# Performance work log

Measured on AMD Instinct MI355X. Metric: run time of the kernel, lower is better.

The kernel has to match this reference:

```python
import jax, jax.numpy as jnp
import numpy as np

B, S, HID = 1, 2048, 2048
NH = 16
D_NOPE, D_ROPE, D_V = 128, 64, 128
D_QK = D_NOPE + D_ROPE            # 192
KV_R = 512                        # kv_lora_rank
EPS = 1e-6
SCALING = D_QK ** -0.5
NEG = -1e9


def rms_norm(x, w):
    xf = x.astype(jnp.float32)
    var = jnp.mean(xf * xf, axis=-1, keepdims=True)
    return w * (xf * jax.lax.rsqrt(var + EPS)).astype(x.dtype)


def rotate_half(x):
    x1, x2 = jnp.split(x, 2, axis=-1)
    return jnp.concatenate([-x2, x1], axis=-1)


def deinterleave(x):
    # torch: view(..., d//2, 2).transpose(-1, -2).reshape(..., d)
    # => [x0, x2, x4, ..., x1, x3, x5, ...]
    return jnp.concatenate([x[..., 0::2], x[..., 1::2]], axis=-1)


def setup_inputs() -> dict:
    key = jax.random.key(0)
    ks = jax.random.split(key, 6)
    hidden_states = jax.random.normal(ks[0], (B, S, HID), jnp.float32)
    # rotary cos/sin over qk_rope_head_dim
    inv_freq = 1.0 / (10000.0 ** (np.arange(0, D_ROPE, 2, dtype=np.float32) / D_ROPE))
    freqs = np.outer(np.arange(S, dtype=np.float32), inv_freq)   # [S, D_ROPE/2]
    emb = np.concatenate([freqs, freqs], axis=-1)                # [S, D_ROPE]
    cos = jnp.asarray(np.cos(emb), jnp.float32)[None]            # [1, S, D_ROPE]
    sin = jnp.asarray(np.sin(emb), jnp.float32)[None]
    # additive causal mask [1, 1, S, S]
    causal = np.where(np.tril(np.ones((S, S), dtype=bool)), 0.0, NEG).astype(np.float32)
    attention_mask = jnp.asarray(causal)[None, None]
    sc = lambda k, shp: jax.random.normal(k, shp, jnp.float32) * (shp[-1] ** -0.5)
    q_proj_w = sc(ks[1], (NH * D_QK, HID))
    kv_a_proj_w = sc(ks[2], (KV_R + D_ROPE, HID))
    kv_a_ln_w = jnp.ones((KV_R,), jnp.float32)
    kv_b_proj_w = sc(ks[3], (NH * (D_NOPE + D_V), KV_R))
    o_proj_w = sc(ks[4], (HID, NH * D_V))
    return dict(hidden_states=hidden_states, cos=cos, sin=sin,
                attention_mask=attention_mask, q_proj_w=q_proj_w,
                kv_a_proj_w=kv_a_proj_w, kv_a_ln_w=kv_a_ln_w,
                kv_b_proj_w=kv_b_proj_w, o_proj_w=o_proj_w)


def reference(hidden_states, cos, sin, attention_mask,
              q_proj_w, kv_a_proj_w, kv_a_ln_w, kv_b_proj_w, o_proj_w):
    b, s, _ = hidden_states.shape
    # Q projection -> [b, NH, s, D_QK]
    q = (hidden_states @ q_proj_w.T).reshape(b, s, NH, D_QK).transpose(0, 2, 1, 3)
    q_pass, q_rot = q[..., :D_NOPE], q[..., D_NOPE:]
    # compressed KV + shared rope key
    ckv = hidden_states @ kv_a_proj_w.T                           # [b, s, KV_R + D_ROPE]
    k_pass_c, k_rot = ckv[..., :KV_R], ckv[..., KV_R:]
    kv = (rms_norm(k_pass_c, kv_a_ln_w) @ kv_b_proj_w.T)
    kv = kv.reshape(b, s, NH, D_NOPE + D_V).transpose(0, 2, 1, 3)  # [b, NH, s, .]
    k_pass, value_states = kv[..., :D_NOPE], kv[..., D_NOPE:]
    k_rot = k_rot.reshape(b, 1, s, D_ROPE)
    # interleaved RoPE (rope_interleave=True)
    q_rot = deinterleave(q_rot)
    k_rot = deinterleave(k_rot)
    c = cos[:, None]  # [1, 1, s, D_ROPE]
    sn = sin[:, None]
    q_rot = q_rot * c + rotate_half(q_rot) * sn
    k_rot = k_rot * c + rotate_half(k_rot) * sn
    k_rot = jnp.broadcast_to(k_rot, (b, NH, s, D_ROPE))
    query_states = jnp.concatenate([q_pass, q_rot], axis=-1)      # [b, NH, s, D_QK]
    key_states = jnp.concatenate([k_pass, k_rot], axis=-1)
    # eager attention (num_key_value_groups == 1)
    scores = jnp.einsum('bhqd,bhkd->bhqk', query_states, key_states) * SCALING
    scores = scores + attention_mask[:, :, :, :s]
    attn = jax.nn.softmax(scores.astype(jnp.float32), axis=-1).astype(query_states.dtype)
    attn_out = jnp.einsum('bhqk,bhkd->bhqd', attn, value_states)  # [b, NH, s, D_V]
    attn_out = attn_out.transpose(0, 2, 1, 3).reshape(b, s, NH * D_V)
    return attn_out @ o_proj_w.T
```

## Files before the change

### kernel.cpp

```cpp
#include <hip/hip_runtime.h>
#include <hip/hip_bf16.h>
#include <stdint.h>
#include <stddef.h>

#define S_LEN 2048
#define HID_DIM 2048
#define NH 16
#define D_QK 192
#define D_NOPE 128
#define D_ROPE 64
#define D_V 128
#define KV_R 512
#define CKV_N (KV_R + D_ROPE)
#define KVB_N (NH * (D_NOPE + D_V))
#define QN (NH * D_QK)
#define CAT_N (QN + CKV_N)
#define SCALING 0.07216878364870322f

typedef __attribute__((ext_vector_type(8))) short short8;
typedef __attribute__((ext_vector_type(4))) short short4v;
typedef __attribute__((ext_vector_type(4))) float f32x4;

__device__ __forceinline__ short f2bf_bits(float f) {
  unsigned u = __float_as_uint(f);
  unsigned r = (u + 0x7fffu + ((u >> 16) & 1u)) >> 16;
  return (short)(r & 0xffffu);
}
__device__ __forceinline__ float bf2f(short b) {
  return __uint_as_float(((unsigned)(unsigned short)b) << 16);
}

__device__ __forceinline__ f32x4 mfma_bf16(short8 a, short8 b, f32x4 c) {
  return __builtin_amdgcn_mfma_f32_16x16x32_bf16(a, b, c, 0, 0, 0);
}

__global__ __launch_bounds__(256)
void cvt5_k(const float* __restrict__ s0, short* __restrict__ d0, int c0,
            const float* __restrict__ s1, short* __restrict__ d1, int c1,
            const float* __restrict__ s2, short* __restrict__ d2, int c2,
            const float* __restrict__ s3, short* __restrict__ d3, int c3,
            const float* __restrict__ s4, short* __restrict__ d4, int c4) {
  const int i = blockIdx.x * 256 + threadIdx.x;
  const float* s; short* d; int base;
  if      (i < c0) { s = s0; d = d0; base = 0;  }
  else if (i < c1) { s = s1; d = d1; base = c0; }
  else if (i < c2) { s = s2; d = d2; base = c1; }
  else if (i < c3) { s = s3; d = d3; base = c2; }
  else if (i < c4) { s = s4; d = d4; base = c3; }
  else return;
  const int j = i - base;
  const float4 v = ((const float4*)s)[j];
  short4v o;
  o.x = f2bf_bits(v.x); o.y = f2bf_bits(v.y);
  o.z = f2bf_bits(v.z); o.w = f2bf_bits(v.w);
  ((short4v*)d)[j] = o;
}

template <bool OUTF32>
__global__ __launch_bounds__(256, 3)
void gemm_bt(const short* __restrict__ A, const short* __restrict__ B,
             void* __restrict__ Cv, int M, int N, int K) {
  __shared__ short sA[2][128 * 32];
  __shared__ short sB[2][128 * 32];
  const int tid  = threadIdx.x;
  const int wave = tid >> 6;
  const int lane = tid & 63;
  const int bm = blockIdx.y * 128;
  const int bn = blockIdx.x * 128;
  const int wr = wave >> 1, wc = wave & 1;
  const int fr = lane & 15, fk = (lane >> 4) * 8;
  const int srow = lane >> 2;
  const int scol = (lane & 3) * 8;

  f32x4 acc[4][4];
  for (int i = 0; i < 4; ++i)
    for (int j = 0; j < 4; ++j)
      for (int r = 0; r < 4; ++r) acc[i][j][r] = 0.f;

  for (int k0 = 0; k0 < K; k0 += 64) {
    __syncthreads();
#pragma unroll
    for (int cc = 0; cc < 2; ++cc) {
      const int c = wave * 2 + cc;
      const int ar = bm + c * 16 + srow;
      int br = bn + c * 16 + srow; if (br > N - 1) br = N - 1;
#pragma unroll
      for (int kh = 0; kh < 2; ++kh) {
        __builtin_amdgcn_global_load_lds(
            (const __attribute__((address_space(1))) void*)(A + (size_t)ar * K + k0 + kh * 32 + scol),
            (__attribute__((address_space(3))) void*)(sA[kh] + c * 512), 16, 0, 0);
        __builtin_amdgcn_global_load_lds(
            (const __attribute__((address_space(1))) void*)(B + (size_t)br * K + k0 + kh * 32 + scol),
            (__attribute__((address_space(3))) void*)(sB[kh] + c * 512), 16, 0, 0);
      }
    }
    __syncthreads();
#pragma unroll
    for (int kh = 0; kh < 2; ++kh) {
      short8 af[4], bfr[4];
#pragma unroll
      for (int i = 0; i < 4; ++i)
        af[i] = *(const short8*)(sA[kh] + (wr * 64 + i * 16 + fr) * 32 + fk);
#pragma unroll
      for (int j = 0; j < 4; ++j)
        bfr[j] = *(const short8*)(sB[kh] + (wc * 64 + j * 16 + fr) * 32 + fk);
#pragma unroll
      for (int i = 0; i < 4; ++i)
#pragma unroll
        for (int j = 0; j < 4; ++j)
          acc[i][j] = mfma_bf16(af[i], bfr[j], acc[i][j]);
    }
  }

  const int cr = (lane >> 4) * 4, ccol = lane & 15;
#pragma unroll
  for (int i = 0; i < 4; ++i)
#pragma unroll
    for (int j = 0; j < 4; ++j) {
      const int col = bn + wc * 64 + j * 16 + ccol;
      if (col < N) {
#pragma unroll
        for (int r = 0; r < 4; ++r) {
          const int row = bm + wr * 64 + i * 16 + cr + r;
          if (OUTF32)
            ((float*)Cv)[(size_t)row * N + col] = acc[i][j][r];
          else
            ((short*)Cv)[(size_t)row * N + col] = f2bf_bits(acc[i][j][r]);
        }
      }
    }
}

__global__ __launch_bounds__(256)
void rmsnorm_k(const short* __restrict__ qckv, const float* __restrict__ w,
               short* __restrict__ out) {
  const int s = blockIdx.x, t = threadIdx.x;
  const short* x = qckv + (size_t)s * CAT_N + QN;
  float v0 = bf2f(x[2 * t]), v1 = bf2f(x[2 * t + 1]);
  float ss = v0 * v0 + v1 * v1;
#pragma unroll
  for (int off = 1; off < 64; off <<= 1) ss += __shfl_xor(ss, off, 64);
  __shared__ float red[4];
  if ((t & 63) == 0) red[t >> 6] = ss;
  __syncthreads();
  const float tot = red[0] + red[1] + red[2] + red[3];
  const float sc = rsqrtf(tot * (1.0f / 512.0f) + 1e-6f);
  out[(size_t)s * KV_R + 2 * t]     = f2bf_bits(v0 * sc * w[2 * t]);
  out[(size_t)s * KV_R + 2 * t + 1] = f2bf_bits(v1 * sc * w[2 * t + 1]);
}

__global__ __launch_bounds__(256)
void prep_k(const short* __restrict__ qckv, const short* __restrict__ kvb,
            const float* __restrict__ cosb, const float* __restrict__ sinb,
            short* __restrict__ Qs, short* __restrict__ Ks) {
  const int s = blockIdx.x, t = threadIdx.x;
  const short* qrow = qckv + (size_t)s * CAT_N;
  __shared__ float cs[32], sn[32];
  __shared__ short krs[64];
  if (t < 32) {
    const float c  = cosb[(size_t)s * 64 + t];
    const float si = sinb[(size_t)s * 64 + t];
    cs[t] = c; sn[t] = si;
    const float e0 = bf2f(qrow[QN + KV_R + 2 * t]);
    const float e1 = bf2f(qrow[QN + KV_R + 2 * t + 1]);
    krs[t]      = f2bf_bits(e0 * c - e1 * si);
    krs[t + 32] = f2bf_bits(e1 * c + e0 * si);
  }
  __syncthreads();
  const int h = t >> 4, i = t & 15;
  *(short8*)(Qs + ((size_t)h * S_LEN + s) * D_QK + i * 8) =
      *(const short8*)(qrow + h * D_QK + i * 8);
  *(short8*)(Ks + ((size_t)h * S_LEN + s) * D_QK + i * 8) =
      *(const short8*)(kvb + (size_t)s * KVB_N + h * 256 + i * 8);
#pragma unroll
  for (int p = 0; p < 2; ++p) {
    const int ii = i * 2 + p;
    const float e0 = bf2f(qrow[h * D_QK + 128 + 2 * ii]);
    const float e1 = bf2f(qrow[h * D_QK + 128 + 2 * ii + 1]);
    Qs[((size_t)h * S_LEN + s) * D_QK + 128 + ii] = f2bf_bits(e0 * cs[ii] - e1 * sn[ii]);
    Qs[((size_t)h * S_LEN + s) * D_QK + 160 + ii] = f2bf_bits(e1 * cs[ii] + e0 * sn[ii]);
  }
#pragma unroll
  for (int p = 0; p < 4; ++p) {
    const int idx = t * 4 + p;
    const int hh = idx >> 6, ii = idx & 63;
    Ks[((size_t)hh * S_LEN + s) * D_QK + 128 + ii] = krs[ii];
  }
}

__global__ __launch_bounds__(256)
void vtr_k(const short* __restrict__ kvb, short* __restrict__ Vt) {
  const int st = blockIdx.x, dt = blockIdx.y, h = blockIdx.z;
  __shared__ short sT[64][72];
  const int id = threadIdx.x;
#pragma unroll
  for (int p = 0; p < 2; ++p) {
    const int q = id + p * 256;
    const int row = q >> 3, c8 = q & 7;
    *(short8*)(&sT[row][c8 * 8]) =
        *(const short8*)(kvb + (size_t)(st * 64 + row) * KVB_N + h * 256 + 128 + dt * 64 + c8 * 8);
  }
  __syncthreads();
#pragma unroll
  for (int p = 0; p < 2; ++p) {
    const int q = id + p * 256;
    const int drow = q >> 3, c8 = q & 7;
    short8 o;
#pragma unroll
    for (int j = 0; j < 8; ++j) o[j] = sT[c8 * 8 + j][drow];
    *(short8*)(Vt + ((size_t)h * D_V + dt * 64 + drow) * S_LEN + st * 64 + c8 * 8) = o;
  }
}

__global__ __launch_bounds__(256, 2)
void flash_k(const short* __restrict__ Qs, const short* __restrict__ Ks,
             const short* __restrict__ Vt, short* __restrict__ Oc) {
  __shared__ short sK[64 * 200];
  __shared__ short sVt[128 * 72];
  __shared__ short P_lds[4][16 * 72];
  const int tid = threadIdx.x;
  const int wv = tid >> 6;
  const int lane = tid & 63;
  const int blk = blockIdx.x;
  const int h = ((blk & 7) << 1) | ((blk >> 3) & 1);
  const int a = blk >> 4;
  const int b = 31 - a;
  const int fr = lane & 15, g = lane >> 4;
  const int q0[2] = { a * 64 + wv * 16, b * 64 + wv * 16 };

  const short* Qh = Qs + (size_t)h * S_LEN * D_QK;
  const short* Kh = Ks + (size_t)h * S_LEN * D_QK;
  const short* Vh = Vt + (size_t)h * D_V * S_LEN;

  short8 qa[2][6];
#pragma unroll
  for (int rt = 0; rt < 2; ++rt)
#pragma unroll
    for (int c = 0; c < 6; ++c)
      qa[rt][c] = *(const short8*)(Qh + (size_t)(q0[rt] + fr) * D_QK + c * 32 + g * 8);

  f32x4 o[2][8];
  float m_i[2][4], l_i[2][4];
#pragma unroll
  for (int rt = 0; rt < 2; ++rt)
#pragma unroll
    for (int r = 0; r < 4; ++r) {
      m_i[rt][r] = -1e30f; l_i[rt][r] = 0.f;
#pragma unroll
      for (int f = 0; f < 8; ++f) o[rt][f][r] = 0.f;
    }

  short* pl = &P_lds[wv][0];
  const int jn = b + 1;
  for (int jt = 0; jt < jn; ++jt) {
    const int j0 = jt << 6;
    const bool lightOn = (jt <= a);
    __syncthreads();
    short8 kc[6], vc[4];
#pragma unroll
    for (int p = 0; p < 6; ++p) {
      const int id = tid + p * 256;
      const int row = id / 24, c8 = id % 24;
      kc[p] = *(const short8*)(Kh + (size_t)(j0 + row) * D_QK + c8 * 8);
    }
#pragma unroll
    for (int p = 0; p < 4; ++p) {
      const int id = tid + p * 256;
      const int row = id >> 3, c8 = id & 7;
      vc[p] = *(const short8*)(Vh + (size_t)row * S_LEN + j0 + c8 * 8);
    }
#pragma unroll
    for (int p = 0; p < 6; ++p) {
      const int id = tid + p * 256;
      const int row = id / 24, c8 = id % 24;
      *(short8*)(sK + row * 200 + c8 * 8) = kc[p];
    }
#pragma unroll
    for (int p = 0; p < 4; ++p) {
      const int id = tid + p * 256;
      const int row = id >> 3, c8 = id & 7;
      *(short8*)(sVt + row * 72 + c8 * 8) = vc[p];
    }
    __syncthreads();

    f32x4 sc[2][4];
#pragma unroll
    for (int rt = 0; rt < 2; ++rt)
#pragma unroll
      for (int t = 0; t < 4; ++t)
        for (int r = 0; r < 4; ++r) sc[rt][t][r] = -1e30f;
#pragma unroll
    for (int t = 0; t < 4; ++t) {
      const bool hOn = (j0 + t * 16 <= q0[1] + 15);
      const bool lOn = lightOn && (j0 + t * 16 <= q0[0] + 15);
      if (hOn || lOn) {
        short8 kfr[6];
#pragma unroll
        for (int c = 0; c < 6; ++c)
          kfr[c] = *(const short8*)(sK + (t * 16 + fr) * 200 + c * 32 + g * 8);
        if (lOn) {
          f32x4 acc; for (int r = 0; r < 4; ++r) acc[r] = 0.f;
#pragma unroll
          for (int c = 0; c < 6; ++c) acc = mfma_bf16(qa[0][c], kfr[c], acc);
          sc[0][t] = acc;
        }
        if (hOn) {
          f32x4 acc; for (int r = 0; r < 4; ++r) acc[r] = 0.f;
#pragma unroll
          for (int c = 0; c < 6; ++c) acc = mfma_bf16(qa[1][c], kfr[c], acc);
          sc[1][t] = acc;
        }
      }
    }

#pragma unroll
    for (int rt = 0; rt < 2; ++rt) {
      if (rt == 0 && !lightOn) continue;
      const int qq = q0[rt];
      float tm[4];
#pragma unroll
      for (int r = 0; r < 4; ++r) {
        const int row = qq + g * 4 + r;
        float mx = -1e30f;
#pragma unroll
        for (int t = 0; t < 4; ++t) {
          const float v = (j0 + t * 16 + fr <= row) ? sc[rt][t][r] * SCALING : -1e30f;
          sc[rt][t][r] = v;
          mx = fmaxf(mx, v);
        }
        tm[r] = mx;
      }
#pragma unroll
      for (int off = 1; off < 16; off <<= 1)
#pragma unroll
        for (int r = 0; r < 4; ++r)
          tm[r] = fmaxf(tm[r], __shfl_xor(tm[r], off, 16));
      float ps[4];
#pragma unroll
      for (int r = 0; r < 4; ++r) {
        const float mnew = fmaxf(m_i[rt][r], tm[r]);
        const float alpha = __expf(m_i[rt][r] - mnew);
        m_i[rt][r] = mnew;
        l_i[rt][r] *= alpha;
        float s = 0.f;
#pragma unroll
        for (int t = 0; t < 4; ++t) {
          const float p = __expf(sc[rt][t][r] - mnew);
          sc[rt][t][r] = p;
          s += p;
        }
        ps[r] = s;
#pragma unroll
        for (int f = 0; f < 8; ++f) o[rt][f][r] *= alpha;
      }
#pragma unroll
      for (int off = 1; off < 16; off <<= 1)
#pragma unroll
        for (int r = 0; r < 4; ++r)
          ps[r] += __shfl_xor(ps[r], off, 16);
#pragma unroll
      for (int r = 0; r < 4; ++r) l_i[rt][r] += ps[r];

#pragma unroll
      for (int r = 0; r < 4; ++r)
#pragma unroll
        for (int t = 0; t < 4; ++t)
          pl[(g * 4 + r) * 72 + t * 16 + fr] = f2bf_bits(sc[rt][t][r]);
      __builtin_amdgcn_fence(__ATOMIC_ACQ_REL, "wavefront");
      const short8 pa0 = *(const short8*)(pl + fr * 72 + g * 8);
      const short8 pa1 = *(const short8*)(pl + fr * 72 + 32 + g * 8);
#pragma unroll
      for (int f = 0; f < 8; ++f) {
        const short* vr = sVt + (f * 16 + fr) * 72 + g * 8;
        const short8 vb0 = *(const short8*)(vr);
        const short8 vb1 = *(const short8*)(vr + 32);
        o[rt][f] = mfma_bf16(pa1, vb1, mfma_bf16(pa0, vb0, o[rt][f]));
      }
    }
  }

#pragma unroll
  for (int rt = 0; rt < 2; ++rt)
#pragma unroll
    for (int r = 0; r < 4; ++r) {
      const float inv = 1.0f / l_i[rt][r];
      const int row = q0[rt] + g * 4 + r;
#pragma unroll
      for (int f = 0; f < 8; ++f)
        Oc[(size_t)row * (NH * D_V) + h * D_V + f * 16 + fr] = f2bf_bits(o[rt][f][r] * inv);
    }
}

extern "C" void kernel_launch(void* const* d_in, const int* in_sizes, int n_in,
                              void* d_out, int out_size, void* d_ws, size_t ws_size,
                              hipStream_t stream) {
  const float* hidden = (const float*)d_in[0];
  const float* cosb   = (const float*)d_in[1];
  const float* sinb   = (const float*)d_in[2];
  const float* q_w    = (const float*)d_in[4];
  const float* kva_w  = (const float*)d_in[5];
  const float* ln_w   = (const float*)d_in[6];
  const float* kvb_w  = (const float*)d_in[7];
  const float* o_w    = (const float*)d_in[8];
  float* out = (float*)d_out;

  char* ws = (char*)d_ws;
  size_t off = 0;
  auto alloc = [&](size_t elems) {
    short* p = (short*)(ws + off);
    off += ((elems * 2 + 255) & ~(size_t)255);
    return p;
  };
  short* hid_b   = alloc((size_t)S_LEN * HID_DIM);
  short* qkva_wb = alloc((size_t)CAT_N * HID_DIM);
  short* kvb_wb  = alloc((size_t)KVB_N * KV_R);
  short* o_wb    = alloc((size_t)HID_DIM * NH * D_V);
  short* qckv    = alloc((size_t)S_LEN * CAT_N);
  short* ckvn    = alloc((size_t)S_LEN * KV_R);
  short* kvb     = alloc((size_t)S_LEN * KVB_N);
  short* Qs      = alloc((size_t)NH * S_LEN * D_QK);
  short* Ks      = alloc((size_t)NH * S_LEN * D_QK);
  short* Vt      = alloc((size_t)NH * D_V * S_LEN);
  short* Oc      = alloc((size_t)S_LEN * NH * D_V);

  dim3 blk(256);
  const int n0 = (S_LEN * HID_DIM) / 4;
  const int n1 = (QN * HID_DIM) / 4;
  const int n2 = (CKV_N * HID_DIM) / 4;
  const int n3 = (KVB_N * KV_R) / 4;
  const int n4e = (HID_DIM * NH * D_V) / 4;
  const int c0 = n0, c1 = c0 + n1, c2 = c1 + n2, c3 = c2 + n3, c4 = c3 + n4e;
  cvt5_k<<<dim3((c4 + 255) / 256), blk, 0, stream>>>(
      hidden, hid_b, c0,
      q_w, qkva_wb, c1,
      kva_w, qkva_wb + (size_t)QN * HID_DIM, c2,
      kvb_w, kvb_wb, c3,
      o_w, o_wb, c4);

  gemm_bt<false><<<dim3((CAT_N + 127) / 128, S_LEN / 128), blk, 0, stream>>>(
      hid_b, qkva_wb, qckv, S_LEN, CAT_N, HID_DIM);
  rmsnorm_k<<<dim3(S_LEN), blk, 0, stream>>>(qckv, ln_w, ckvn);
  gemm_bt<false><<<dim3(KVB_N / 128, S_LEN / 128), blk, 0, stream>>>(
      ckvn, kvb_wb, kvb, S_LEN, KVB_N, KV_R);
  prep_k<<<dim3(S_LEN), blk, 0, stream>>>(qckv, kvb, cosb, sinb, Qs, Ks);
  vtr_k<<<dim3(S_LEN / 64, D_V / 64, NH), blk, 0, stream>>>(kvb, Vt);
  flash_k<<<dim3(NH * 16), blk, 0, stream>>>(Qs, Ks, Vt, Oc);
  gemm_bt<true><<<dim3(HID_DIM / 128, S_LEN / 128), blk, 0, stream>>>(
      Oc, o_wb, out, S_LEN, HID_DIM, NH * D_V);
}
```

Measured before the change: 320.1 us.

## Prefetch next K/V tile into registers during flash attention compute

Issues the global loads for the next K and V tiles into registers right after the shared-memory barrier, so they are in flight while the current tile's QK^T, softmax and PV run. The following iteration only copies those registers into LDS. Per-thread row and column indices are precomputed once, and launch bounds drop from 2 to 1 blocks per CU so the extra live registers do not cause spills. The cost is lower occupancy, which may hide latency less well than running two blocks per CU.

```diff
diff --git a/kernel.cpp b/kernel.cpp
--- a/kernel.cpp
+++ b/kernel.cpp
@@ -212,7 +212,7 @@
   }
 }
 
-__global__ __launch_bounds__(256, 2)
+__global__ __launch_bounds__(256, 1)
 void flash_k(const short* __restrict__ Qs, const short* __restrict__ Ks,
              const short* __restrict__ Vt, short* __restrict__ Oc) {
   __shared__ short sK[64 * 200];
@@ -232,6 +232,18 @@
   const short* Kh = Ks + (size_t)h * S_LEN * D_QK;
   const short* Vh = Vt + (size_t)h * D_V * S_LEN;
 
+  int rowK[6], c8K[6], rowV[4], c8V[4];
+#pragma unroll
+  for (int p = 0; p < 6; ++p) {
+    const int id = tid + p * 256;
+    rowK[p] = id / 24; c8K[p] = id % 24;
+  }
+#pragma unroll
+  for (int p = 0; p < 4; ++p) {
+    const int id = tid + p * 256;
+    rowV[p] = id >> 3; c8V[p] = id & 7;
+  }
+
   short8 qa[2][6];
 #pragma unroll
   for (int rt = 0; rt < 2; ++rt)
@@ -249,6 +261,14 @@
 #pragma unroll
       for (int f = 0; f < 8; ++f) o[rt][f][r] = 0.f;
     }
+
+  short8 kc[6], vc[4];
+#pragma unroll
+  for (int p = 0; p < 6; ++p)
+    kc[p] = *(const short8*)(Kh + (size_t)rowK[p] * D_QK + c8K[p] * 8);
+#pragma unroll
+  for (int p = 0; p < 4; ++p)
+    vc[p] = *(const short8*)(Vh + (size_t)rowV[p] * S_LEN + c8V[p] * 8);
 
   short* pl = &P_lds[wv][0];
   const int jn = b + 1;
@@ -256,32 +276,22 @@
     const int j0 = jt << 6;
     const bool lightOn = (jt <= a);
     __syncthreads();
-    short8 kc[6], vc[4];
-#pragma unroll
-    for (int p = 0; p < 6; ++p) {
-      const int id = tid + p * 256;
-      const int row = id / 24, c8 = id % 24;
-      kc[p] = *(const short8*)(Kh + (size_t)(j0 + row) * D_QK + c8 * 8);
-    }
-#pragma unroll
-    for (int p = 0; p < 4; ++p) {
-      const int id = tid + p * 256;
-      const int row = id >> 3, c8 = id & 7;
-      vc[p] = *(const short8*)(Vh + (size_t)row * S_LEN + j0 + c8 * 8);
-    }
-#pragma unroll
-    for (int p = 0; p < 6; ++p) {
-      const int id = tid + p * 256;
-      const int row = id / 24, c8 = id % 24;
-      *(short8*)(sK + row * 200 + c8 * 8) = kc[p];
-    }
-#pragma unroll
-    for (int p = 0; p < 4; ++p) {
-      const int id = tid + p * 256;
-      const int row = id >> 3, c8 = id & 7;
-      *(short8*)(sVt + row * 72 + c8 * 8) = vc[p];
-    }
+#pragma unroll
+    for (int p = 0; p < 6; ++p)
+      *(short8*)(sK + rowK[p] * 200 + c8K[p] * 8) = kc[p];
+#pragma unroll
+    for (int p = 0; p < 4; ++p)
+      *(short8*)(sVt + rowV[p] * 72 + c8V[p] * 8) = vc[p];
     __syncthreads();
+    if (jt + 1 < jn) {
+      const int j1 = (jt + 1) << 6;
+#pragma unroll
+      for (int p = 0; p < 6; ++p)
+        kc[p] = *(const short8*)(Kh + (size_t)(j1 + rowK[p]) * D_QK + c8K[p] * 8);
+#pragma unroll
+      for (int p = 0; p < 4; ++p)
+        vc[p] = *(const short8*)(Vh + (size_t)rowV[p] * S_LEN + j1 + c8V[p] * 8);
+    }
 
     f32x4 sc[2][4];
 #pragma unroll
```

After: 321.1 us. No clear change (+0.3%).
